# Optimization experiments

Measured on AMD Instinct MI355X. Metric: run time of the kernel, lower is better.

Reference implementation:

```python
import jax, jax.numpy as jnp
import numpy as np

N, H, C, A, G, NG = 400000, 256, 128, 32, 512, 1024
BN_EPS = 1e-5


def setup_inputs() -> dict:
    key = jax.random.key(0)
    ks = jax.random.split(key, 14)
    s = lambda fan: 1.0 / np.sqrt(fan)
    return {
        "initial_node_states": jax.random.normal(ks[0], (N, H), jnp.float32),
        "final_node_states": jax.random.normal(ks[1], (N, H), jnp.float32),
        "aux_variables": jax.random.normal(ks[2], (NG, A), jnp.float32),
        "graph_nodes_list": jnp.sort(jax.random.randint(ks[3], (N,), 0, NG, jnp.int32)),
        "num_graphs": NG,
        "Wg": jax.random.normal(ks[4], (2 * H, C), jnp.float32) * s(2 * H),
        "bg": jnp.zeros((C,), jnp.float32),
        "Wt": jax.random.normal(ks[5], (H, C), jnp.float32) * s(H),
        "bt": jnp.zeros((C,), jnp.float32),
        "gamma": jnp.ones((C + A,), jnp.float32),
        "beta": jnp.zeros((C + A,), jnp.float32),
        "W1": jax.random.normal(ks[6], (C + A, G), jnp.float32) * s(C + A),
        "b1": jnp.zeros((G,), jnp.float32),
        "W2": jax.random.normal(ks[7], (G, C), jnp.float32) * s(G),
        "b2": jnp.zeros((C,), jnp.float32),
    }


def reference(initial_node_states, final_node_states, aux_variables,
              graph_nodes_list, num_graphs,
              Wg, bg, Wt, bt, gamma, beta, W1, b1, W2, b2):
    # Nodewise gated readout (dropout layers are identity in eval mode)
    gate_input = jnp.concatenate([initial_node_states, final_node_states], axis=-1)  # [N, 2H]
    gate = jax.nn.sigmoid(gate_input @ Wg + bg)                                      # [N, C]
    nodewise = gate * (final_node_states @ Wt + bt)                                  # [N, C]
    # Scatter-add into per-graph buckets (index_add_)
    graph_readout = jax.ops.segment_sum(nodewise, graph_nodes_list, num_segments=num_graphs)  # [NG, C]
    ext = jnp.concatenate([graph_readout, aux_variables], axis=1)                    # [NG, C+A]
    # BatchNorm1d (training-mode batch statistics, biased variance)
    mean = ext.mean(axis=0)
    var = ext.var(axis=0)
    norm = (ext - mean) / jnp.sqrt(var + BN_EPS) * gamma + beta
    # Small MLP head
    hidden = jax.nn.relu(norm @ W1 + b1)
    logits = hidden @ W2 + b2                                                        # [NG, C]
    return logits
```

## Files before the change

### kernel.cpp

```cpp
#include <hip/hip_runtime.h>
#include <hip/hip_bf16.h>

#define NNODES 400000
#define BM 64

typedef __attribute__((ext_vector_type(8))) short  short8;
typedef __attribute__((ext_vector_type(4))) float  floatx4;

typedef unsigned short u16;
typedef unsigned int   u32;

__device__ __forceinline__ short f2bf(float f) {
    u32 u = __builtin_bit_cast(u32, f);
    u += 0x7fffu + ((u >> 16) & 1u);
    return (short)(u >> 16);
}

__device__ __forceinline__ void async16(const void* g, void* l) {
    __builtin_amdgcn_global_load_lds(
        (const __attribute__((address_space(1))) u32*)g,
        (__attribute__((address_space(3))) u32*)l, 16, 0, 0);
}

__global__ __launch_bounds__(256) void k0_build(
    const float* __restrict__ Wg, const float* __restrict__ Wt,
    u16* __restrict__ Bp)
{
    int base = (blockIdx.x * 256 + threadIdx.x) * 4;
    #pragma unroll
    for (int e = 0; e < 4; e++) {
        int idx   = base + e;
        int local = idx & 4095;
        int quad  = local >> 10;
        int col   = (local >> 3) & 127;
        int j     = local & 7;
        float v;
        if (idx < 65536) {
            int kc = idx >> 12;
            v = Wg[(kc * 32 + quad * 8 + j) * 128 + col];
        } else {
            int kct = (idx - 65536) >> 12;
            v = Wt[(kct * 32 + quad * 8 + j) * 128 + col];
        }
        Bp[idx] = (u16)f2bf(v);
    }
}

__global__ __launch_bounds__(256, 4) void k1_gemm(
    const float* __restrict__ initS, const float* __restrict__ finS,
    const int* __restrict__ gids, const u16* __restrict__ Bp,
    const float* __restrict__ bg, const float* __restrict__ bt,
    float* __restrict__ readout)
{
    __shared__ __align__(16) u16 Bl[2][8192];
    __shared__ int gidL[BM];

    const int tid  = threadIdx.x;
    const int w    = tid >> 6;
    const int lane = tid & 63;
    const int quad = lane >> 4;
    const int l15  = lane & 15;
    const int nodeBase = blockIdx.x * BM;

    if (tid < BM) gidL[tid] = gids[nodeBase + tid];

    floatx4 accg[8], acct[8];
    #pragma unroll
    for (int i = 0; i < 8; i++) {
        accg[i] = (floatx4){0.f, 0.f, 0.f, 0.f};
        acct[i] = (floatx4){0.f, 0.f, 0.f, 0.f};
    }

    const int rowNode = nodeBase + w * 16 + l15;
    const float* initRow = initS + (size_t)rowNode * 256;
    const float* finRow  = finS  + (size_t)rowNode * 256;

    auto stage = [&](int kc, u16* lbuf) {
        if (kc < 8) {
            #pragma unroll
            for (int i = 0; i < 2; i++) {
                int c = w * 2 + i;
                async16(Bp + (size_t)kc * 4096 + c * 512 + lane * 8, lbuf + c * 512);
            }
        } else {
            #pragma unroll
            for (int i = 0; i < 4; i++) {
                int c = w * 4 + i;
                const u16* src = (c < 8)
                    ? (Bp + (size_t)kc * 4096 + c * 512)
                    : (Bp + 65536 + (size_t)(kc - 8) * 4096 + (c - 8) * 512);
                async16(src + lane * 8, lbuf + c * 512);
            }
        }
    };

    stage(0, Bl[0]);
    const float* ar = initRow + quad * 8;
    float4 a0 = *reinterpret_cast<const float4*>(ar);
    float4 a1 = *reinterpret_cast<const float4*>(ar + 4);

    for (int kc = 0; kc < 16; kc++) {
        const u16* cur = Bl[kc & 1];
        __syncthreads();

        float4 a0n, a1n;
        if (kc < 15) {
            stage(kc + 1, Bl[(kc + 1) & 1]);
            const float* arn = ((kc + 1) < 8)
                ? (initRow + (kc + 1) * 32 + quad * 8)
                : (finRow + (kc + 1 - 8) * 32 + quad * 8);
            a0n = *reinterpret_cast<const float4*>(arn);
            a1n = *reinterpret_cast<const float4*>(arn + 4);
        }

        short8 af;
        af[0] = f2bf(a0.x); af[1] = f2bf(a0.y); af[2] = f2bf(a0.z); af[3] = f2bf(a0.w);
        af[4] = f2bf(a1.x); af[5] = f2bf(a1.y); af[6] = f2bf(a1.z); af[7] = f2bf(a1.w);

        #pragma unroll
        for (int ct = 0; ct < 8; ct++) {
            short8 bf = *reinterpret_cast<const short8*>(
                cur + quad * 1024 + (ct * 16 + l15) * 8);
            accg[ct] = __builtin_amdgcn_mfma_f32_16x16x32_bf16(af, bf, accg[ct], 0, 0, 0);
        }
        if (kc >= 8) {
            #pragma unroll
            for (int ct = 0; ct < 8; ct++) {
                short8 bf = *reinterpret_cast<const short8*>(
                    cur + 4096 + quad * 1024 + (ct * 16 + l15) * 8);
                acct[ct] = __builtin_amdgcn_mfma_f32_16x16x32_bf16(af, bf, acct[ct], 0, 0, 0);
            }
        }
        a0 = a0n; a1 = a1n;
    }

    const int rbase = w * 16;
    const int gFirst = gidL[rbase];
    const int gLast  = gidL[rbase + 15];

    if (gFirst == gLast) {
        #pragma unroll
        for (int ct = 0; ct < 8; ct++) {
            const float bgv = bg[ct * 16 + l15];
            const float btv = bt[ct * 16 + l15];
            float s = 0.f;
            #pragma unroll
            for (int i = 0; i < 4; i++) {
                float g = accg[ct][i] + bgv;
                float t = acct[ct][i] + btv;
                s += t / (1.0f + __expf(-g));
            }
            s += __shfl_xor(s, 16);
            s += __shfl_xor(s, 32);
            if ((ct >> 1) == quad)
                atomicAdd(&readout[gFirst * 128 + ct * 16 + l15], s);
        }
    } else {
        float s[8];
        #pragma unroll
        for (int ct = 0; ct < 8; ct++) s[ct] = 0.f;
        int curg = gidL[rbase + quad * 4];
        #pragma unroll
        for (int i = 0; i < 4; i++) {
            int g = gidL[rbase + quad * 4 + i];
            if (g != curg) {
                #pragma unroll
                for (int ct = 0; ct < 8; ct++) {
                    atomicAdd(&readout[curg * 128 + ct * 16 + l15], s[ct]);
                    s[ct] = 0.f;
                }
                curg = g;
            }
            #pragma unroll
            for (int ct = 0; ct < 8; ct++) {
                float gg = accg[ct][i] + bg[ct * 16 + l15];
                float tt = acct[ct][i] + bt[ct * 16 + l15];
                s[ct] += tt / (1.0f + __expf(-gg));
            }
        }
        #pragma unroll
        for (int ct = 0; ct < 8; ct++)
            atomicAdd(&readout[curg * 128 + ct * 16 + l15], s[ct]);
    }
}

__global__ __launch_bounds__(256) void k2_stats(
    const float* __restrict__ readout, const float* __restrict__ aux,
    const float* __restrict__ gamma, const float* __restrict__ beta,
    float* __restrict__ scale, float* __restrict__ shift)
{
    const int col = blockIdx.x;
    const int tid = threadIdx.x;
    float s = 0.f, q = 0.f;
    for (int g = tid; g < 1024; g += 256) {
        float v = (col < 128) ? readout[g * 128 + col] : aux[g * 32 + (col - 128)];
        s += v; q += v * v;
    }
    #pragma unroll
    for (int off = 32; off > 0; off >>= 1) {
        s += __shfl_down(s, off);
        q += __shfl_down(q, off);
    }
    __shared__ float ps[4], pq[4];
    if ((tid & 63) == 0) { ps[tid >> 6] = s; pq[tid >> 6] = q; }
    __syncthreads();
    if (tid == 0) {
        float S = ps[0] + ps[1] + ps[2] + ps[3];
        float Q = pq[0] + pq[1] + pq[2] + pq[3];
        float mean = S * (1.0f / 1024.0f);
        float var  = Q * (1.0f / 1024.0f) - mean * mean;
        float rstd = rsqrtf(var + 1e-5f);
        float sc   = gamma[col] * rstd;
        scale[col] = sc;
        shift[col] = beta[col] - mean * sc;
    }
}

__global__ __launch_bounds__(256) void k3a_hidden(
    const float* __restrict__ readout, const float* __restrict__ aux,
    const float* __restrict__ scale, const float* __restrict__ shift,
    const float* __restrict__ W1, const float* __restrict__ b1,
    float* __restrict__ hidden)
{
    const int g0  = blockIdx.x * 4;
    const int tid = threadIdx.x;
    const float* r0 = readout + (size_t)g0 * 128;
    const float* a0 = aux     + (size_t)g0 * 32;

    #pragma unroll
    for (int jj = 0; jj < 2; jj++) {
        const int j = tid + jj * 256;
        float acc0 = 0.f, acc1 = 0.f, acc2 = 0.f, acc3 = 0.f, accS = 0.f;
        for (int k = 0; k < 128; k++) {
            float wv = W1[k * 512 + j];
            accS += shift[k] * wv;
            float wsv = scale[k] * wv;
            acc0 += r0[k]       * wsv;
            acc1 += r0[128 + k] * wsv;
            acc2 += r0[256 + k] * wsv;
            acc3 += r0[384 + k] * wsv;
        }
        for (int k = 0; k < 32; k++) {
            float wv = W1[(128 + k) * 512 + j];
            accS += shift[128 + k] * wv;
            float wsv = scale[128 + k] * wv;
            acc0 += a0[k]      * wsv;
            acc1 += a0[32 + k] * wsv;
            acc2 += a0[64 + k] * wsv;
            acc3 += a0[96 + k] * wsv;
        }
        float bb = b1[j] + accS;
        hidden[(size_t)(g0 + 0) * 512 + j] = fmaxf(acc0 + bb, 0.f);
        hidden[(size_t)(g0 + 1) * 512 + j] = fmaxf(acc1 + bb, 0.f);
        hidden[(size_t)(g0 + 2) * 512 + j] = fmaxf(acc2 + bb, 0.f);
        hidden[(size_t)(g0 + 3) * 512 + j] = fmaxf(acc3 + bb, 0.f);
    }
}

__global__ __launch_bounds__(256) void k3b_logits(
    const float* __restrict__ hidden, const float* __restrict__ W2,
    const float* __restrict__ b2, float* __restrict__ out)
{
    const int g0  = blockIdx.x * 4;
    const int tid = threadIdx.x;
    const int j   = tid & 127;
    const int rh  = tid >> 7;
    const float* h0 = hidden + (size_t)(g0 + rh * 2) * 512;
    float acc0 = 0.f, acc1 = 0.f;
    for (int k = 0; k < 512; k++) {
        float wv = W2[k * 128 + j];
        acc0 += h0[k]       * wv;
        acc1 += h0[512 + k] * wv;
    }
    float bb = b2[j];
    out[(size_t)(g0 + rh * 2 + 0) * 128 + j] = acc0 + bb;
    out[(size_t)(g0 + rh * 2 + 1) * 128 + j] = acc1 + bb;
}

extern "C" void kernel_launch(void* const* d_in, const int* in_sizes, int n_in,
                              void* d_out, int out_size, void* d_ws, size_t ws_size,
                              hipStream_t stream)
{
    const float* initS = (const float*)d_in[0];
    const float* finS  = (const float*)d_in[1];
    const float* aux   = (const float*)d_in[2];
    const int*   gid   = (const int*)d_in[3];
    const float* Wg    = (const float*)d_in[5];
    const float* bg    = (const float*)d_in[6];
    const float* Wt    = (const float*)d_in[7];
    const float* bt    = (const float*)d_in[8];
    const float* gamma = (const float*)d_in[9];
    const float* beta  = (const float*)d_in[10];
    const float* W1    = (const float*)d_in[11];
    const float* b1    = (const float*)d_in[12];
    const float* W2    = (const float*)d_in[13];
    const float* b2    = (const float*)d_in[14];
    float* out = (float*)d_out;

    char* ws = (char*)d_ws;
    u16*   Bp      = (u16*)(ws + 0);
    float* readout = (float*)(ws + 262144);
    float* scale   = (float*)(ws + 786432);
    float* shift   = (float*)(ws + 787456);
    float* hidden  = (float*)(ws + 1048576);

    k0_build  <<<96, 256, 0, stream>>>(Wg, Wt, Bp);
    hipMemsetAsync(readout, 0, 1024 * 128 * sizeof(float), stream);
    k1_gemm   <<<NNODES / BM, 256, 0, stream>>>(initS, finS, gid, Bp, bg, bt, readout);
    k2_stats  <<<160, 256, 0, stream>>>(readout, aux, gamma, beta, scale, shift);
    k3a_hidden<<<256, 256, 0, stream>>>(readout, aux, scale, shift, W1, b1, hidden);
    k3b_logits<<<256, 256, 0, stream>>>(hidden, W2, b2, out);
}
```

Baseline: 926.8 us.

## Read packed bf16 weights directly from global memory instead of LDS staging

The GEMM kernel no longer stages the packed Wg/Wt bf16 weights into double-buffered shared memory through async global-to-LDS loads. Each lane now loads its B fragments straight from global memory, relying on L1/L2 caching of the small weight matrix. Graph ids also move from shared memory into registers and are broadcast with lane shuffles. This removes LDS traffic, the LDS footprint and most of the synchronisation, which may allow higher occupancy, at the cost of more global/L1 load requests and longer latency per MFMA operand.

New measurement: 1.013 ms. 1.09x slower.

```diff
diff --git a/kernel.cpp b/kernel.cpp
--- a/kernel.cpp
+++ b/kernel.cpp
@@ -14,12 +14,6 @@
     u32 u = __builtin_bit_cast(u32, f);
     u += 0x7fffu + ((u >> 16) & 1u);
     return (short)(u >> 16);
-}
-
-__device__ __forceinline__ void async16(const void* g, void* l) {
-    __builtin_amdgcn_global_load_lds(
-        (const __attribute__((address_space(1))) u32*)g,
-        (__attribute__((address_space(3))) u32*)l, 16, 0, 0);
 }
 
 __global__ __launch_bounds__(256) void k0_build(
@@ -52,9 +46,6 @@
     const float* __restrict__ bg, const float* __restrict__ bt,
     float* __restrict__ readout)
 {
-    __shared__ __align__(16) u16 Bl[2][8192];
-    __shared__ int gidL[BM];
-
     const int tid  = threadIdx.x;
     const int w    = tid >> 6;
     const int lane = tid & 63;
@@ -62,7 +53,8 @@
     const int l15  = lane & 15;
     const int nodeBase = blockIdx.x * BM;
 
-    if (tid < BM) gidL[tid] = gids[nodeBase + tid];
+    const int rowNode = nodeBase + w * 16 + l15;
+    const int myg = gids[rowNode];
 
     floatx4 accg[8], acct[8];
     #pragma unroll
@@ -71,41 +63,21 @@
         acct[i] = (floatx4){0.f, 0.f, 0.f, 0.f};
     }
 
-    const int rowNode = nodeBase + w * 16 + l15;
     const float* initRow = initS + (size_t)rowNode * 256;
     const float* finRow  = finS  + (size_t)rowNode * 256;
 
-    auto stage = [&](int kc, u16* lbuf) {
-        if (kc < 8) {
-            #pragma unroll
-            for (int i = 0; i < 2; i++) {
-                int c = w * 2 + i;
-                async16(Bp + (size_t)kc * 4096 + c * 512 + lane * 8, lbuf + c * 512);
-            }
-        } else {
-            #pragma unroll
-            for (int i = 0; i < 4; i++) {
-                int c = w * 4 + i;
-                const u16* src = (c < 8)
-                    ? (Bp + (size_t)kc * 4096 + c * 512)
-                    : (Bp + 65536 + (size_t)(kc - 8) * 4096 + (c - 8) * 512);
-                async16(src + lane * 8, lbuf + c * 512);
-            }
-        }
-    };
-
-    stage(0, Bl[0]);
+    const u16* BgBase = Bp + quad * 1024 + l15 * 8;
+    const u16* BtBase = Bp + 65536 + quad * 1024 + l15 * 8;
+
     const float* ar = initRow + quad * 8;
     float4 a0 = *reinterpret_cast<const float4*>(ar);
     float4 a1 = *reinterpret_cast<const float4*>(ar + 4);
 
     for (int kc = 0; kc < 16; kc++) {
-        const u16* cur = Bl[kc & 1];
-        __syncthreads();
+        __builtin_amdgcn_s_barrier();
 
         float4 a0n, a1n;
         if (kc < 15) {
-            stage(kc + 1, Bl[(kc + 1) & 1]);
             const float* arn = ((kc + 1) < 8)
                 ? (initRow + (kc + 1) * 32 + quad * 8)
                 : (finRow + (kc + 1 - 8) * 32 + quad * 8);
@@ -117,26 +89,25 @@
         af[0] = f2bf(a0.x); af[1] = f2bf(a0.y); af[2] = f2bf(a0.z); af[3] = f2bf(a0.w);
         af[4] = f2bf(a1.x); af[5] = f2bf(a1.y); af[6] = f2bf(a1.z); af[7] = f2bf(a1.w);
 
+        const u16* bgp = BgBase + (size_t)kc * 4096;
         #pragma unroll
         for (int ct = 0; ct < 8; ct++) {
-            short8 bf = *reinterpret_cast<const short8*>(
-                cur + quad * 1024 + (ct * 16 + l15) * 8);
+            short8 bf = *reinterpret_cast<const short8*>(bgp + ct * 128);
             accg[ct] = __builtin_amdgcn_mfma_f32_16x16x32_bf16(af, bf, accg[ct], 0, 0, 0);
         }
         if (kc >= 8) {
+            const u16* btp = BtBase + (size_t)(kc - 8) * 4096;
             #pragma unroll
             for (int ct = 0; ct < 8; ct++) {
-                short8 bf = *reinterpret_cast<const short8*>(
-                    cur + 4096 + quad * 1024 + (ct * 16 + l15) * 8);
+                short8 bf = *reinterpret_cast<const short8*>(btp + ct * 128);
                 acct[ct] = __builtin_amdgcn_mfma_f32_16x16x32_bf16(af, bf, acct[ct], 0, 0, 0);
             }
         }
         a0 = a0n; a1 = a1n;
     }
 
-    const int rbase = w * 16;
-    const int gFirst = gidL[rbase];
-    const int gLast  = gidL[rbase + 15];
+    const int gFirst = __shfl(myg, 0);
+    const int gLast  = __shfl(myg, 15);
 
     if (gFirst == gLast) {
         #pragma unroll
@@ -159,10 +130,10 @@
         float s[8];
         #pragma unroll
         for (int ct = 0; ct < 8; ct++) s[ct] = 0.f;
-        int curg = gidL[rbase + quad * 4];
+        int curg = __shfl(myg, quad * 4);
         #pragma unroll
         for (int i = 0; i < 4; i++) {
-            int g = gidL[rbase + quad * 4 + i];
+            int g = __shfl(myg, quad * 4 + i);
             if (g != curg) {
                 #pragma unroll
                 for (int ct = 0; ct < 8; ct++) {
```
